# Optimization experiments

Hardware: AMD Instinct MI355X
Metric: run time of the kernel (lower is better)

## Reference

```python
import jax, jax.numpy as jnp
import numpy as np

D_MODEL = 384
HEAD_SIZE = 64
B, T = 64, 512


def setup_inputs() -> dict:
    key = jax.random.key(0)
    kx, kq, kk, kv = jax.random.split(key, 4)
    x = jax.random.normal(kx, (B, T, D_MODEL), dtype=jnp.float32)
    Wq = jax.random.normal(kq, (D_MODEL, HEAD_SIZE), dtype=jnp.float32) * 0.02
    Wk = jax.random.normal(kk, (D_MODEL, HEAD_SIZE), dtype=jnp.float32) * 0.02
    Wv = jax.random.normal(kv, (D_MODEL, HEAD_SIZE), dtype=jnp.float32) * 0.02
    return {"x": x, "Wq": Wq, "Wk": Wk, "Wv": Wv}


def reference(x, Wq, Wk, Wv):
    # x: [B, T, C]; projections (bias-free linear layers)
    q = jnp.einsum("btc,ch->bth", x, Wq)  # [B, T, H]
    k = jnp.einsum("btc,ch->bth", x, Wk)
    v = jnp.einsum("btc,ch->bth", x, Wv)
    Tn = x.shape[1]
    scale = 1.0 / jnp.sqrt(jnp.float32(k.shape[-1]))
    wei = jnp.einsum("bqh,bkh->bqk", q, k) * scale  # [B, T, T]
    causal = jnp.tril(jnp.ones((Tn, Tn), dtype=bool))
    wei = jnp.where(causal, wei, -jnp.inf)
    wei = jax.nn.softmax(wei, axis=-1)
    # dropout omitted (eval mode) for deterministic reference
    out = jnp.einsum("bqk,bkh->bqh", wei, v)  # [B, T, H]
    return out
```

## Files before the change

### kernel.cpp

```cpp
#include <hip/hip_runtime.h>
#include <math.h>

#define NB 64
#define NT 512
#define NC 384
#define NH 64

typedef __attribute__((ext_vector_type(8))) short bf16x8;
typedef __attribute__((ext_vector_type(4))) float f32x4;

__device__ __forceinline__ unsigned short f2bf(float f) {
  unsigned int u = __float_as_uint(f);
  unsigned int r = (u + 0x7FFFu + ((u >> 16) & 1u)) >> 16;
  return (unsigned short)r;
}

__global__ __launch_bounds__(256) void wtrans_kernel(
    const float* __restrict__ Wq, const float* __restrict__ Wk,
    const float* __restrict__ Wv, unsigned short* __restrict__ Wt) {
  int id = blockIdx.x * 256 + threadIdx.x;
  if (id >= 3 * NC * NH) return;
  int m = id / (NC * NH);
  int r = id % (NC * NH);
  int c = r / NH;
  int h = r % NH;
  const float* W = (m == 0) ? Wq : ((m == 1) ? Wk : Wv);
  Wt[(m * NH + h) * NC + c] = f2bf(W[c * NH + h]);
}

#define XS 392
#define WS 40
__global__ __launch_bounds__(256) void proj_kernel(
    const float* __restrict__ x, const unsigned short* __restrict__ Wt,
    unsigned short* __restrict__ qkv) {
  __shared__ unsigned short xs[64 * XS];
  __shared__ unsigned short ws[192 * WS];
  const int t = threadIdx.x;
  const int m0 = blockIdx.x * 64;
  const int w = t >> 6, l = t & 63, mi = l & 15, quad = l >> 4;

  for (int i = 0; i < 24; ++i) {
    int u = t + i * 256;
    int row = u / 96;
    int cp = (u % 96) * 4;
    const float* src = x + (size_t)(m0 + row) * NC + cp;
    float4 a = *(const float4*)src;
    ushort4 bb;
    bb.x = f2bf(a.x); bb.y = f2bf(a.y); bb.z = f2bf(a.z); bb.w = f2bf(a.w);
    *(ushort4*)&xs[row * XS + cp] = bb;
  }

  f32x4 acc[12];
  const f32x4 zero = {0.f, 0.f, 0.f, 0.f};
#pragma unroll
  for (int i = 0; i < 12; ++i) acc[i] = zero;

  for (int kc = 0; kc < 12; ++kc) {
    const int c0 = kc * 32;
    __syncthreads();
#pragma unroll
    for (int i = 0; i < 3; ++i) {
      int u = t + i * 256;
      int row = u >> 2;
      int seg = u & 3;
      *(uint4*)&ws[row * WS + seg * 8] =
          *(const uint4*)&Wt[row * NC + c0 + seg * 8];
    }
    __syncthreads();
    bf16x8 a = *(const bf16x8*)&xs[(w * 16 + mi) * XS + c0 + quad * 8];
#pragma unroll
    for (int nt = 0; nt < 12; ++nt) {
      bf16x8 b = *(const bf16x8*)&ws[(nt * 16 + mi) * WS + quad * 8];
      acc[nt] = __builtin_amdgcn_mfma_f32_16x16x32_bf16(a, b, acc[nt], 0, 0, 0);
    }
  }

#pragma unroll
  for (int nt = 0; nt < 12; ++nt) {
    int n = nt * 16 + mi;
    int mat = n >> 6;
    int h = n & 63;
    unsigned short* dst = qkv + (size_t)mat * (32768 * 64);
#pragma unroll
    for (int r = 0; r < 4; ++r) {
      int row = m0 + w * 16 + quad * 4 + r;
      dst[(size_t)row * NH + h] = f2bf(acc[nt][r]);
    }
  }
}

#define AS 72
__global__ __launch_bounds__(256) void attn_kernel(
    const unsigned short* __restrict__ q, const unsigned short* __restrict__ k,
    const unsigned short* __restrict__ v, float* __restrict__ out) {
  __shared__ unsigned short qs[64 * AS];
  __shared__ unsigned short ks[64 * AS];
  __shared__ unsigned short vts[64 * AS];
  __shared__ unsigned short ps[64 * AS];

  const int t = threadIdx.x;
  const int bx = blockIdx.x;
  const int qt = 7 - (bx >> 6);
  const int b = bx & 63;
  const int w = t >> 6, l = t & 63, mi = l & 15, quad = l >> 4;

  const size_t qbase = ((size_t)b * NT + qt * 64) * NH;
#pragma unroll
  for (int i = 0; i < 2; ++i) {
    int u = t + i * 256;
    int row = u >> 3, seg = u & 7;
    *(uint4*)&qs[row * AS + seg * 8] = *(const uint4*)&q[qbase + row * 64 + seg * 8];
  }

  f32x4 accO[4];
  const f32x4 zero = {0.f, 0.f, 0.f, 0.f};
#pragma unroll
  for (int i = 0; i < 4; ++i) accO[i] = zero;
  float mrow[4], lrow[4];
#pragma unroll
  for (int r = 0; r < 4; ++r) { mrow[r] = -INFINITY; lrow[r] = 0.f; }

  for (int kt = 0; kt <= qt; ++kt) {
    const size_t kbase = ((size_t)b * NT + kt * 64) * NH;
    __syncthreads();
#pragma unroll
    for (int i = 0; i < 2; ++i) {
      int u = t + i * 256;
      int row = u >> 3, seg = u & 7;
      *(uint4*)&ks[row * AS + seg * 8] = *(const uint4*)&k[kbase + row * 64 + seg * 8];
    }
    {
      int row = t >> 2;
      int h0 = (t & 3) * 16;
      unsigned short tmp[16];
      *(uint4*)&tmp[0] = *(const uint4*)&v[kbase + row * 64 + h0];
      *(uint4*)&tmp[8] = *(const uint4*)&v[kbase + row * 64 + h0 + 8];
#pragma unroll
      for (int i = 0; i < 16; ++i) vts[(h0 + i) * AS + row] = tmp[i];
    }
    __syncthreads();

    f32x4 s[4];
    bf16x8 a0 = *(const bf16x8*)&qs[(w * 16 + mi) * AS + quad * 8];
    bf16x8 a1 = *(const bf16x8*)&qs[(w * 16 + mi) * AS + 32 + quad * 8];
#pragma unroll
    for (int nt = 0; nt < 4; ++nt) {
      bf16x8 b0 = *(const bf16x8*)&ks[(nt * 16 + mi) * AS + quad * 8];
      bf16x8 b1 = *(const bf16x8*)&ks[(nt * 16 + mi) * AS + 32 + quad * 8];
      f32x4 z = zero;
      z = __builtin_amdgcn_mfma_f32_16x16x32_bf16(a0, b0, z, 0, 0, 0);
      z = __builtin_amdgcn_mfma_f32_16x16x32_bf16(a1, b1, z, 0, 0, 0);
      s[nt] = z;
    }
#pragma unroll
    for (int nt = 0; nt < 4; ++nt)
#pragma unroll
      for (int r = 0; r < 4; ++r) s[nt][r] *= 0.125f;

    if (kt == qt) {
#pragma unroll
      for (int nt = 0; nt < 4; ++nt) {
        int key = nt * 16 + mi;
#pragma unroll
        for (int r = 0; r < 4; ++r) {
          int qrow = w * 16 + quad * 4 + r;
          if (key > qrow) s[nt][r] = -INFINITY;
        }
      }
    }

    float alpha[4];
#pragma unroll
    for (int r = 0; r < 4; ++r) {
      float v0 = fmaxf(fmaxf(s[0][r], s[1][r]), fmaxf(s[2][r], s[3][r]));
      v0 = fmaxf(v0, __shfl_xor(v0, 1));
      v0 = fmaxf(v0, __shfl_xor(v0, 2));
      v0 = fmaxf(v0, __shfl_xor(v0, 4));
      v0 = fmaxf(v0, __shfl_xor(v0, 8));
      float mn = fmaxf(mrow[r], v0);
      alpha[r] = __expf(mrow[r] - mn);
      mrow[r] = mn;
    }
    float rs[4] = {0.f, 0.f, 0.f, 0.f};
#pragma unroll
    for (int nt = 0; nt < 4; ++nt) {
#pragma unroll
      for (int r = 0; r < 4; ++r) {
        float p = __expf(s[nt][r] - mrow[r]);
        rs[r] += p;
        ps[(w * 16 + quad * 4 + r) * AS + nt * 16 + mi] = f2bf(p);
      }
    }
#pragma unroll
    for (int r = 0; r < 4; ++r) {
      float v0 = rs[r];
      v0 += __shfl_xor(v0, 1);
      v0 += __shfl_xor(v0, 2);
      v0 += __shfl_xor(v0, 4);
      v0 += __shfl_xor(v0, 8);
      lrow[r] = lrow[r] * alpha[r] + v0;
    }
#pragma unroll
    for (int nt = 0; nt < 4; ++nt)
#pragma unroll
      for (int r = 0; r < 4; ++r) accO[nt][r] *= alpha[r];

    __syncthreads();

    bf16x8 pa0 = *(const bf16x8*)&ps[(w * 16 + mi) * AS + quad * 8];
    bf16x8 pa1 = *(const bf16x8*)&ps[(w * 16 + mi) * AS + 32 + quad * 8];
#pragma unroll
    for (int nt = 0; nt < 4; ++nt) {
      bf16x8 vb0 = *(const bf16x8*)&vts[(nt * 16 + mi) * AS + quad * 8];
      bf16x8 vb1 = *(const bf16x8*)&vts[(nt * 16 + mi) * AS + 32 + quad * 8];
      accO[nt] = __builtin_amdgcn_mfma_f32_16x16x32_bf16(pa0, vb0, accO[nt], 0, 0, 0);
      accO[nt] = __builtin_amdgcn_mfma_f32_16x16x32_bf16(pa1, vb1, accO[nt], 0, 0, 0);
    }
  }

  const size_t obase = ((size_t)b * NT + qt * 64) * NH;
#pragma unroll
  for (int nt = 0; nt < 4; ++nt) {
#pragma unroll
    for (int r = 0; r < 4; ++r) {
      out[obase + (size_t)(w * 16 + quad * 4 + r) * NH + nt * 16 + mi] =
          accO[nt][r] / lrow[r];
    }
  }
}

extern "C" void kernel_launch(void* const* d_in, const int* in_sizes, int n_in,
                              void* d_out, int out_size, void* d_ws, size_t ws_size,
                              hipStream_t stream) {
  const float* x  = (const float*)d_in[0];
  const float* Wq = (const float*)d_in[1];
  const float* Wk = (const float*)d_in[2];
  const float* Wv = (const float*)d_in[3];

  unsigned short* Wt = (unsigned short*)d_ws;
  unsigned short* qb = Wt + 192 * 384;
  unsigned short* kb = qb + 32768 * 64;
  unsigned short* vb = kb + 32768 * 64;
  float* out = (float*)d_out;

  wtrans_kernel<<<288, 256, 0, stream>>>(Wq, Wk, Wv, Wt);
  proj_kernel<<<512, 256, 0, stream>>>(x, Wt, qb);
  attn_kernel<<<512, 256, 0, stream>>>(qb, kb, vb, out);
}
```

Measured before the change: 123.1 us.

## Store V transposed from projection, compute S transposed, keep Q in registers

The projection kernel now writes V in a per-batch transposed layout, folds the 1/sqrt(d) scale into Q, and reads weights straight from global memory instead of staging them in shared memory. The attention kernel loads Q fragments directly into registers and computes the transposed score tile, so each lane owns one query row. Softmax reductions then need only two cross-lane shuffles, and P is written to LDS as packed row fragments, which removes one block barrier per key tile. The V transpose through LDS scatter is replaced by plain vector copies. The cost is uncoalesced strided global writes for V-transposed and weight reads from global/L2 in the projection.

```diff
diff --git a/kernel.cpp b/kernel.cpp
--- a/kernel.cpp
+++ b/kernel.cpp
@@ -11,8 +11,10 @@
 
 __device__ __forceinline__ unsigned short f2bf(float f) {
   unsigned int u = __float_as_uint(f);
-  unsigned int r = (u + 0x7FFFu + ((u >> 16) & 1u)) >> 16;
-  return (unsigned short)r;
+  return (unsigned short)((u + 0x7FFFu + ((u >> 16) & 1u)) >> 16);
+}
+__device__ __forceinline__ unsigned int pk2bf(float a, float b) {
+  return (unsigned int)f2bf(a) | ((unsigned int)f2bf(b) << 16);
 }
 
 __global__ __launch_bounds__(256) void wtrans_kernel(
@@ -29,12 +31,11 @@
 }
 
 #define XS 392
-#define WS 40
 __global__ __launch_bounds__(256) void proj_kernel(
     const float* __restrict__ x, const unsigned short* __restrict__ Wt,
-    unsigned short* __restrict__ qkv) {
+    unsigned short* __restrict__ q, unsigned short* __restrict__ k,
+    unsigned short* __restrict__ vt) {
   __shared__ unsigned short xs[64 * XS];
-  __shared__ unsigned short ws[192 * WS];
   const int t = threadIdx.x;
   const int m0 = blockIdx.x * 64;
   const int w = t >> 6, l = t & 63, mi = l & 15, quad = l >> 4;
@@ -43,12 +44,12 @@
     int u = t + i * 256;
     int row = u / 96;
     int cp = (u % 96) * 4;
-    const float* src = x + (size_t)(m0 + row) * NC + cp;
-    float4 a = *(const float4*)src;
+    float4 a = *(const float4*)(x + (size_t)(m0 + row) * NC + cp);
     ushort4 bb;
     bb.x = f2bf(a.x); bb.y = f2bf(a.y); bb.z = f2bf(a.z); bb.w = f2bf(a.w);
     *(ushort4*)&xs[row * XS + cp] = bb;
   }
+  __syncthreads();
 
   f32x4 acc[12];
   const f32x4 zero = {0.f, 0.f, 0.f, 0.f};
@@ -56,21 +57,11 @@
   for (int i = 0; i < 12; ++i) acc[i] = zero;
 
   for (int kc = 0; kc < 12; ++kc) {
-    const int c0 = kc * 32;
-    __syncthreads();
-#pragma unroll
-    for (int i = 0; i < 3; ++i) {
-      int u = t + i * 256;
-      int row = u >> 2;
-      int seg = u & 3;
-      *(uint4*)&ws[row * WS + seg * 8] =
-          *(const uint4*)&Wt[row * NC + c0 + seg * 8];
-    }
-    __syncthreads();
-    bf16x8 a = *(const bf16x8*)&xs[(w * 16 + mi) * XS + c0 + quad * 8];
+    bf16x8 a = *(const bf16x8*)&xs[(w * 16 + mi) * XS + kc * 32 + quad * 8];
+    const unsigned short* wp = Wt + (size_t)mi * NC + kc * 32 + quad * 8;
 #pragma unroll
     for (int nt = 0; nt < 12; ++nt) {
-      bf16x8 b = *(const bf16x8*)&ws[(nt * 16 + mi) * WS + quad * 8];
+      bf16x8 b = *(const bf16x8*)(wp + (size_t)nt * 16 * NC);
       acc[nt] = __builtin_amdgcn_mfma_f32_16x16x32_bf16(a, b, acc[nt], 0, 0, 0);
     }
   }
@@ -80,11 +71,21 @@
     int n = nt * 16 + mi;
     int mat = n >> 6;
     int h = n & 63;
-    unsigned short* dst = qkv + (size_t)mat * (32768 * 64);
-#pragma unroll
-    for (int r = 0; r < 4; ++r) {
-      int row = m0 + w * 16 + quad * 4 + r;
-      dst[(size_t)row * NH + h] = f2bf(acc[nt][r]);
+    if (mat < 2) {
+      unsigned short* dst = (mat == 0) ? q : k;
+      float sc = (mat == 0) ? 0.125f : 1.0f;
+#pragma unroll
+      for (int r = 0; r < 4; ++r) {
+        int row = m0 + w * 16 + quad * 4 + r;
+        dst[(size_t)row * NH + h] = f2bf(acc[nt][r] * sc);
+      }
+    } else {
+#pragma unroll
+      for (int r = 0; r < 4; ++r) {
+        int row = m0 + w * 16 + quad * 4 + r;
+        int bb = row >> 9, tt = row & 511;
+        vt[((size_t)bb * NH + h) * NT + tt] = f2bf(acc[nt][r]);
+      }
     }
   }
 }
@@ -92,8 +93,7 @@
 #define AS 72
 __global__ __launch_bounds__(256) void attn_kernel(
     const unsigned short* __restrict__ q, const unsigned short* __restrict__ k,
-    const unsigned short* __restrict__ v, float* __restrict__ out) {
-  __shared__ unsigned short qs[64 * AS];
+    const unsigned short* __restrict__ vt, float* __restrict__ out) {
   __shared__ unsigned short ks[64 * AS];
   __shared__ unsigned short vts[64 * AS];
   __shared__ unsigned short ps[64 * AS];
@@ -105,126 +105,110 @@
   const int w = t >> 6, l = t & 63, mi = l & 15, quad = l >> 4;
 
   const size_t qbase = ((size_t)b * NT + qt * 64) * NH;
-#pragma unroll
-  for (int i = 0; i < 2; ++i) {
-    int u = t + i * 256;
-    int row = u >> 3, seg = u & 7;
-    *(uint4*)&qs[row * AS + seg * 8] = *(const uint4*)&q[qbase + row * 64 + seg * 8];
-  }
+  const unsigned short* qrow = q + qbase + (size_t)(w * 16 + mi) * NH;
+  bf16x8 qb0 = *(const bf16x8*)(qrow + quad * 8);
+  bf16x8 qb1 = *(const bf16x8*)(qrow + 32 + quad * 8);
 
   f32x4 accO[4];
   const f32x4 zero = {0.f, 0.f, 0.f, 0.f};
 #pragma unroll
   for (int i = 0; i < 4; ++i) accO[i] = zero;
-  float mrow[4], lrow[4];
-#pragma unroll
-  for (int r = 0; r < 4; ++r) { mrow[r] = -INFINITY; lrow[r] = 0.f; }
+  float mrow = -INFINITY, lrow = 0.f;
 
   for (int kt = 0; kt <= qt; ++kt) {
     const size_t kbase = ((size_t)b * NT + kt * 64) * NH;
+    const size_t vtbase = (size_t)b * NH * NT + kt * 64;
     __syncthreads();
 #pragma unroll
     for (int i = 0; i < 2; ++i) {
       int u = t + i * 256;
       int row = u >> 3, seg = u & 7;
-      *(uint4*)&ks[row * AS + seg * 8] = *(const uint4*)&k[kbase + row * 64 + seg * 8];
-    }
-    {
-      int row = t >> 2;
-      int h0 = (t & 3) * 16;
-      unsigned short tmp[16];
-      *(uint4*)&tmp[0] = *(const uint4*)&v[kbase + row * 64 + h0];
-      *(uint4*)&tmp[8] = *(const uint4*)&v[kbase + row * 64 + h0 + 8];
-#pragma unroll
-      for (int i = 0; i < 16; ++i) vts[(h0 + i) * AS + row] = tmp[i];
+      *(uint4*)&ks[row * AS + seg * 8] =
+          *(const uint4*)&k[kbase + row * 64 + seg * 8];
+      *(uint4*)&vts[row * AS + seg * 8] =
+          *(const uint4*)&vt[vtbase + (size_t)row * NT + seg * 8];
     }
     __syncthreads();
 
-    f32x4 s[4];
-    bf16x8 a0 = *(const bf16x8*)&qs[(w * 16 + mi) * AS + quad * 8];
-    bf16x8 a1 = *(const bf16x8*)&qs[(w * 16 + mi) * AS + 32 + quad * 8];
+    float p[4][4];
 #pragma unroll
     for (int nt = 0; nt < 4; ++nt) {
-      bf16x8 b0 = *(const bf16x8*)&ks[(nt * 16 + mi) * AS + quad * 8];
-      bf16x8 b1 = *(const bf16x8*)&ks[(nt * 16 + mi) * AS + 32 + quad * 8];
+      bf16x8 a0 = *(const bf16x8*)&ks[(nt * 16 + mi) * AS + quad * 8];
+      bf16x8 a1 = *(const bf16x8*)&ks[(nt * 16 + mi) * AS + 32 + quad * 8];
       f32x4 z = zero;
-      z = __builtin_amdgcn_mfma_f32_16x16x32_bf16(a0, b0, z, 0, 0, 0);
-      z = __builtin_amdgcn_mfma_f32_16x16x32_bf16(a1, b1, z, 0, 0, 0);
-      s[nt] = z;
-    }
+      z = __builtin_amdgcn_mfma_f32_16x16x32_bf16(a0, qb0, z, 0, 0, 0);
+      z = __builtin_amdgcn_mfma_f32_16x16x32_bf16(a1, qb1, z, 0, 0, 0);
+#pragma unroll
+      for (int r = 0; r < 4; ++r) p[nt][r] = z[r];
+    }
+
+    if (kt == qt) {
+#pragma unroll
+      for (int nt = 0; nt < 4; ++nt)
+#pragma unroll
+        for (int r = 0; r < 4; ++r)
+          if (nt * 16 + quad * 4 + r > w * 16 + mi) p[nt][r] = -INFINITY;
+    }
+
+    float vmax = -INFINITY;
 #pragma unroll
     for (int nt = 0; nt < 4; ++nt)
 #pragma unroll
-      for (int r = 0; r < 4; ++r) s[nt][r] *= 0.125f;
-
-    if (kt == qt) {
-#pragma unroll
-      for (int nt = 0; nt < 4; ++nt) {
-        int key = nt * 16 + mi;
-#pragma unroll
-        for (int r = 0; r < 4; ++r) {
-          int qrow = w * 16 + quad * 4 + r;
-          if (key > qrow) s[nt][r] = -INFINITY;
-        }
+      for (int r = 0; r < 4; ++r) vmax = fmaxf(vmax, p[nt][r]);
+    vmax = fmaxf(vmax, __shfl_xor(vmax, 16));
+    vmax = fmaxf(vmax, __shfl_xor(vmax, 32));
+    float mn = fmaxf(mrow, vmax);
+    float alpha = __expf(mrow - mn);
+    mrow = mn;
+
+    float rsum = 0.f;
+#pragma unroll
+    for (int nt = 0; nt < 4; ++nt)
+#pragma unroll
+      for (int r = 0; r < 4; ++r) {
+        p[nt][r] = __expf(p[nt][r] - mn);
+        rsum += p[nt][r];
       }
-    }
-
-    float alpha[4];
-#pragma unroll
-    for (int r = 0; r < 4; ++r) {
-      float v0 = fmaxf(fmaxf(s[0][r], s[1][r]), fmaxf(s[2][r], s[3][r]));
-      v0 = fmaxf(v0, __shfl_xor(v0, 1));
-      v0 = fmaxf(v0, __shfl_xor(v0, 2));
-      v0 = fmaxf(v0, __shfl_xor(v0, 4));
-      v0 = fmaxf(v0, __shfl_xor(v0, 8));
-      float mn = fmaxf(mrow[r], v0);
-      alpha[r] = __expf(mrow[r] - mn);
-      mrow[r] = mn;
-    }
-    float rs[4] = {0.f, 0.f, 0.f, 0.f};
+    rsum += __shfl_xor(rsum, 16);
+    rsum += __shfl_xor(rsum, 32);
+    lrow = lrow * alpha + rsum;
+
 #pragma unroll
     for (int nt = 0; nt < 4; ++nt) {
-#pragma unroll
-      for (int r = 0; r < 4; ++r) {
-        float p = __expf(s[nt][r] - mrow[r]);
-        rs[r] += p;
-        ps[(w * 16 + quad * 4 + r) * AS + nt * 16 + mi] = f2bf(p);
-      }
-    }
-#pragma unroll
-    for (int r = 0; r < 4; ++r) {
-      float v0 = rs[r];
-      v0 += __shfl_xor(v0, 1);
-      v0 += __shfl_xor(v0, 2);
-      v0 += __shfl_xor(v0, 4);
-      v0 += __shfl_xor(v0, 8);
-      lrow[r] = lrow[r] * alpha[r] + v0;
-    }
-#pragma unroll
-    for (int nt = 0; nt < 4; ++nt)
-#pragma unroll
-      for (int r = 0; r < 4; ++r) accO[nt][r] *= alpha[r];
-
-    __syncthreads();
-
+      uint2 pk;
+      pk.x = pk2bf(p[nt][0], p[nt][1]);
+      pk.y = pk2bf(p[nt][2], p[nt][3]);
+      *(uint2*)&ps[(w * 16 + mi) * AS + nt * 16 + quad * 4] = pk;
+    }
     bf16x8 pa0 = *(const bf16x8*)&ps[(w * 16 + mi) * AS + quad * 8];
     bf16x8 pa1 = *(const bf16x8*)&ps[(w * 16 + mi) * AS + 32 + quad * 8];
-#pragma unroll
-    for (int nt = 0; nt < 4; ++nt) {
-      bf16x8 vb0 = *(const bf16x8*)&vts[(nt * 16 + mi) * AS + quad * 8];
-      bf16x8 vb1 = *(const bf16x8*)&vts[(nt * 16 + mi) * AS + 32 + quad * 8];
-      accO[nt] = __builtin_amdgcn_mfma_f32_16x16x32_bf16(pa0, vb0, accO[nt], 0, 0, 0);
-      accO[nt] = __builtin_amdgcn_mfma_f32_16x16x32_bf16(pa1, vb1, accO[nt], 0, 0, 0);
-    }
-  }
-
+
+    float av[4];
+#pragma unroll
+    for (int r = 0; r < 4; ++r) av[r] = __shfl(alpha, quad * 4 + r);
+#pragma unroll
+    for (int hi = 0; hi < 4; ++hi)
+#pragma unroll
+      for (int r = 0; r < 4; ++r) accO[hi][r] *= av[r];
+
+#pragma unroll
+    for (int hi = 0; hi < 4; ++hi) {
+      bf16x8 vb0 = *(const bf16x8*)&vts[(hi * 16 + mi) * AS + quad * 8];
+      bf16x8 vb1 = *(const bf16x8*)&vts[(hi * 16 + mi) * AS + 32 + quad * 8];
+      accO[hi] = __builtin_amdgcn_mfma_f32_16x16x32_bf16(pa0, vb0, accO[hi], 0, 0, 0);
+      accO[hi] = __builtin_amdgcn_mfma_f32_16x16x32_bf16(pa1, vb1, accO[hi], 0, 0, 0);
+    }
+  }
+
+  float inv = 1.f / lrow;
   const size_t obase = ((size_t)b * NT + qt * 64) * NH;
 #pragma unroll
-  for (int nt = 0; nt < 4; ++nt) {
-#pragma unroll
-    for (int r = 0; r < 4; ++r) {
-      out[obase + (size_t)(w * 16 + quad * 4 + r) * NH + nt * 16 + mi] =
-          accO[nt][r] / lrow[r];
+  for (int r = 0; r < 4; ++r) {
+    float iv = __shfl(inv, quad * 4 + r);
+#pragma unroll
+    for (int hi = 0; hi < 4; ++hi) {
+      out[obase + (size_t)(w * 16 + quad * 4 + r) * NH + hi * 16 + mi] =
+          accO[hi][r] * iv;
     }
   }
 }
@@ -240,10 +224,10 @@
   unsigned short* Wt = (unsigned short*)d_ws;
   unsigned short* qb = Wt + 192 * 384;
   unsigned short* kb = qb + 32768 * 64;
-  unsigned short* vb = kb + 32768 * 64;
+  unsigned short* vtb = kb + 32768 * 64;
   float* out = (float*)d_out;
 
   wtrans_kernel<<<288, 256, 0, stream>>>(Wq, Wk, Wv, Wt);
-  proj_kernel<<<512, 256, 0, stream>>>(x, Wt, qb);
-  attn_kernel<<<512, 256, 0, stream>>>(qb, kb, vb, out);
-}
+  proj_kernel<<<512, 256, 0, stream>>>(x, Wt, qb, kb, vtb);
+  attn_kernel<<<512, 256, 0, stream>>>(qb, kb, vtb, out);
+}
```

Measured after the change: 144.0 us. 1.17x slower.
